# Performance work log

Measured on AMD Instinct MI355X. Metric: run time of the kernel, lower is better.

The kernel has to match this reference:

```python
import jax, jax.numpy as jnp
import numpy as np


def spmm(src, dst, w, x, n):
    # out[i] = sum_{e: dst[e]==i} w[e] * x[src[e]]  == th.spmm(adj, x) with adj COO (dst=row, src=col)
    return jax.ops.segment_sum(x[src] * w[:, None], dst, num_segments=n)


def gcn(x, ei, w, W1, b1, W2, b2):
    # GCN.forward: relu(gc1(x, adj)) -> dropout(eval: identity) -> gc2(x, adj)
    n = x.shape[0]
    src, dst = ei[1], ei[0]
    h = jax.nn.relu(spmm(src, dst, w, x @ W1, n) + b1)
    return spmm(src, dst, w, h @ W2, n) + b2


def setup_inputs() -> dict:
    key = jax.random.key(0)
    ks = jax.random.split(key, 24)
    Nd, Ns = 100000, 50000
    Fd, Fs, H1, H2 = 256, 256, 256, 128
    DEG = 32
    Ed, Es = Nd * DEG, Ns * DEG
    inp = {}
    inp['drug_sim_feat'] = jax.random.normal(ks[0], (Nd, Fd), jnp.float32)
    inp['drug_edge_index'] = jax.random.randint(ks[1], (2, Ed), 0, Nd, jnp.int32)
    inp['drug_edge_weight'] = jax.random.uniform(ks[2], (Ed,), jnp.float32) / DEG
    inp['drug_feat_edge_index'] = jax.random.randint(ks[3], (2, Ed), 0, Nd, jnp.int32)
    inp['drug_feat_edge_weight'] = jax.random.uniform(ks[4], (Ed,), jnp.float32) / DEG
    inp['disease_sim_feat'] = jax.random.normal(ks[5], (Ns, Fs), jnp.float32)
    inp['dis_edge_index'] = jax.random.randint(ks[6], (2, Es), 0, Ns, jnp.int32)
    inp['dis_edge_weight'] = jax.random.uniform(ks[7], (Es,), jnp.float32) / DEG
    inp['dis_feat_edge_index'] = jax.random.randint(ks[8], (2, Es), 0, Ns, jnp.int32)
    inp['dis_feat_edge_weight'] = jax.random.uniform(ks[9], (Es,), jnp.float32) / DEG
    # params: uniform(-stdv, stdv), stdv = 1/sqrt(out_features) as in reset_parameters
    def unif(k, shape, out_f):
        s = 1.0 / np.sqrt(out_f)
        return jax.random.uniform(k, shape, jnp.float32, -s, s)
    inp['W1d'] = unif(ks[10], (Fd, H1), H1); inp['b1d'] = unif(ks[11], (H1,), H1)
    inp['W2d'] = unif(ks[12], (H1, H2), H2); inp['b2d'] = unif(ks[13], (H2,), H2)
    inp['W1s'] = unif(ks[14], (Fs, H1), H1); inp['b1s'] = unif(ks[15], (H1,), H1)
    inp['W2s'] = unif(ks[16], (H1, H2), H2); inp['b2s'] = unif(ks[17], (H2,), H2)
    # fusion Linears (nhid2*2 -> nhid2); kaiming-ish uniform
    fs = 1.0 / np.sqrt(2 * H2)
    inp['Wfd'] = jax.random.uniform(ks[18], (2 * H2, H2), jnp.float32, -fs, fs)
    inp['bfd'] = jax.random.uniform(ks[19], (H2,), jnp.float32, -fs, fs)
    inp['Wfs'] = jax.random.uniform(ks[20], (2 * H2, H2), jnp.float32, -fs, fs)
    inp['bfs'] = jax.random.uniform(ks[21], (H2,), jnp.float32, -fs, fs)
    return inp


def reference(drug_sim_feat, drug_edge_index, drug_edge_weight,
              drug_feat_edge_index, drug_feat_edge_weight,
              disease_sim_feat, dis_edge_index, dis_edge_weight,
              dis_feat_edge_index, dis_feat_edge_weight,
              W1d, b1d, W2d, b2d, W1s, b1s, W2s, b2s,
              Wfd, bfd, Wfs, bfs):
    # dropout in eval mode (identity)
    emb1_sim = gcn(drug_sim_feat, drug_edge_index, drug_edge_weight, W1d, b1d, W2d, b2d)
    emb2_sim = gcn(disease_sim_feat, dis_edge_index, dis_edge_weight, W1s, b1s, W2s, b2s)
    emb1_feat = gcn(drug_sim_feat, drug_feat_edge_index, drug_feat_edge_weight, W1d, b1d, W2d, b2d)
    emb2_feat = gcn(disease_sim_feat, dis_feat_edge_index, dis_feat_edge_weight, W1s, b1s, W2s, b2s)
    emb1 = jax.nn.relu(jnp.concatenate([emb1_sim, emb1_feat], axis=1) @ Wfd + bfd)
    emb2 = jax.nn.relu(jnp.concatenate([emb2_sim, emb2_feat], axis=1) @ Wfs + bfs)
    return (emb1, emb2, emb1_sim, emb1_feat, emb2_sim, emb2_feat)
```

## Files before the change

kernel.cpp:

```cpp
#include <hip/hip_runtime.h>

typedef _Float16 f16;
typedef __attribute__((ext_vector_type(8))) _Float16 f16x8;
typedef __attribute__((ext_vector_type(4))) float f32x4;

__device__ inline ushort f2h_bits(float f) {
    f16 h = (f16)f;
    return __builtin_bit_cast(ushort, h);
}

__global__ __launch_bounds__(256) void f2h_vec(const float* __restrict__ in,
                                               ushort* __restrict__ out, int n4) {
    for (int i = blockIdx.x * 256 + threadIdx.x; i < n4; i += gridDim.x * 256) {
        float4 v = reinterpret_cast<const float4*>(in)[i];
        reinterpret_cast<ushort4*>(out)[i] =
            make_ushort4(f2h_bits(v.x), f2h_bits(v.y), f2h_bits(v.z), f2h_bits(v.w));
    }
}

__global__ __launch_bounds__(256) void transpose_f16_k(const float* __restrict__ W,
                                                       ushort* __restrict__ Wt,
                                                       int K, int N) {
    __shared__ ushort tile[32][33];
    int k0 = blockIdx.x * 32, n0 = blockIdx.y * 32;
    int tx = threadIdx.x & 31, ty = threadIdx.x >> 5;
    #pragma unroll
    for (int i = 0; i < 32; i += 8)
        tile[ty + i][tx] = f2h_bits(W[(size_t)(k0 + ty + i) * N + n0 + tx]);
    __syncthreads();
    #pragma unroll
    for (int i = 0; i < 32; i += 8)
        Wt[(size_t)(n0 + ty + i) * K + k0 + tx] = tile[tx][ty + i];
}


__global__ __launch_bounds__(256) void bucket_hist(const int* __restrict__ dst, int E,
                                                   int* __restrict__ counts) {
    __shared__ int h[512];
    int t = threadIdx.x;
    h[t] = 0; h[t + 256] = 0;
    __syncthreads();
    int e0 = blockIdx.x * 4096;
    #pragma unroll
    for (int k = 0; k < 16; ++k) {
        int i = e0 + t + k * 256;
        if (i < E) atomicAdd(&h[((uint)dst[i]) >> 8], 1);
    }
    __syncthreads();
    for (int b = t; b < 512; b += 256)
        if (h[b]) atomicAdd(&counts[b], h[b]);
}

__global__ __launch_bounds__(256) void bucket_scan(const int* __restrict__ counts, int NB, int E,
                                                   int* __restrict__ base, int* __restrict__ cursor,
                                                   int* __restrict__ row_ptr, int n) {
    int t = threadIdx.x, lane = t & 63, wave = t >> 6;
    int v0 = (2 * t     < NB) ? counts[2 * t]     : 0;
    int v1 = (2 * t + 1 < NB) ? counts[2 * t + 1] : 0;
    int s = v0 + v1;
    int incl = s;
    for (int off = 1; off < 64; off <<= 1) {
        int u = __shfl_up(incl, off);
        if (lane >= off) incl += u;
    }
    __shared__ int wsum[4];
    if (lane == 63) wsum[wave] = incl;
    __syncthreads();
    int excl = incl - s;
    for (int wv = 0; wv < wave; ++wv) excl += wsum[wv];
    if (2 * t < NB)     { base[2 * t]     = excl;      cursor[2 * t]     = excl; }
    if (2 * t + 1 < NB) { base[2 * t + 1] = excl + v0; cursor[2 * t + 1] = excl + v0; }
    if (t == 0) { base[NB] = E; row_ptr[n] = E; }
}

__global__ __launch_bounds__(256) void scatter_binned(const int* __restrict__ ei,
                                                      const float* __restrict__ w, int E,
                                                      int* __restrict__ bucket_cursor,
                                                      int2* __restrict__ bst) {
    __shared__ int hist[512], excl[512], sbase[512], lcur[512];
    __shared__ int2 stage[4096];
    __shared__ ushort sbin[4096];
    const int t = threadIdx.x, lane = t & 63, wave = t >> 6;
    const int e0 = blockIdx.x * 4096;
    const int cnt = min(4096, E - e0);

    hist[t] = 0; hist[t + 256] = 0;
    __syncthreads();

    int   d[16], s[16];
    float wv[16];
    #pragma unroll
    for (int k = 0; k < 16; ++k) {
        int i = t + k * 256;
        if (i < cnt) {
            d[k]  = ei[e0 + i];
            s[k]  = ei[(size_t)E + e0 + i];
            wv[k] = w[e0 + i];
            atomicAdd(&hist[((uint)d[k]) >> 8], 1);
        }
    }
    __syncthreads();

    {
        int v0 = hist[2 * t], v1 = hist[2 * t + 1];
        int sum = v0 + v1;
        int incl = sum;
        for (int off = 1; off < 64; off <<= 1) {
            int u = __shfl_up(incl, off);
            if (lane >= off) incl += u;
        }
        __shared__ int wsum[4];
        if (lane == 63) wsum[wave] = incl;
        __syncthreads();
        int e = incl - sum;
        for (int wvv = 0; wvv < wave; ++wvv) e += wsum[wvv];
        excl[2 * t] = e; excl[2 * t + 1] = e + v0;
    }
    __syncthreads();

    for (int b = t; b < 512; b += 256) {
        int c = hist[b];
        sbase[b] = c ? atomicAdd(&bucket_cursor[b], c) : 0;
        lcur[b] = excl[b];
    }
    __syncthreads();

    #pragma unroll
    for (int k = 0; k < 16; ++k) {
        int i = t + k * 256;
        if (i < cnt) {
            int bin = ((uint)d[k]) >> 8;
            int pos = atomicAdd(&lcur[bin], 1);
            stage[pos] = make_int2((s[k] << 8) | (d[k] & 255), __float_as_int(wv[k]));
            sbin[pos] = (ushort)bin;
        }
    }
    __syncthreads();

    #pragma unroll
    for (int k = 0; k < 16; ++k) {
        int i = t + k * 256;
        if (i < cnt) {
            int2 r = stage[i];
            int bin = sbin[i];
            bst[(size_t)sbase[bin] + i - excl[bin]] = r;
        }
    }
}

__global__ __launch_bounds__(256) void bucket_finalize(const int2* __restrict__ bst,
                                                       const int* __restrict__ base,
                                                       int* __restrict__ row_ptr,
                                                       int2* __restrict__ perm, int n) {
    __shared__ int hist[256], cur[256], wsum[4];
    const int b = blockIdx.x, t = threadIdx.x, lane = t & 63, wave = t >> 6;
    const int lo = base[b], hi = base[b + 1];
    hist[t] = 0;
    __syncthreads();
    for (int i = lo + t; i < hi; i += 256)
        atomicAdd(&hist[bst[i].x & 255], 1);
    __syncthreads();
    int v = hist[t];
    int incl = v;
    for (int off = 1; off < 64; off <<= 1) {
        int u = __shfl_up(incl, off);
        if (lane >= off) incl += u;
    }
    if (lane == 63) wsum[wave] = incl;
    __syncthreads();
    int excl = incl - v;
    for (int wv = 0; wv < wave; ++wv) excl += wsum[wv];
    const int r0 = b << 8;
    const int nrows = min(256, n - r0);
    if (t < nrows) row_ptr[r0 + t] = lo + excl;
    cur[t] = lo + excl;
    __syncthreads();
    for (int i = lo + t; i < hi; i += 256) {
        int2 r = bst[i];
        int local = r.x & 255;
        int slot = atomicAdd(&cur[local], 1);
        perm[slot] = make_int2(r.x >> 8, r.y);
    }
}

template<int C, bool RELU, bool DUAL>
__global__ __launch_bounds__(256) void spmm_f16(
    const f16* __restrict__ x,
    const int2* __restrict__ perm,
    const int* __restrict__ row_ptr, const float* __restrict__ bias,
    ushort* __restrict__ out_h, float* __restrict__ out_f, int n)
{
    const int wave = threadIdx.x >> 6, lane = threadIdx.x & 63;
    const int row = blockIdx.x * 4 + wave;
    if (row >= n) return;
    const int F = 64 * C;
    const int e0 = row_ptr[row], e1 = row_ptr[row + 1];
    float acc[C] = {};
    const int laneoff = lane * C;

    for (int eb = e0; eb < e1; eb += 64) {
        int idx = eb + lane;
        int myS = 0; int myW = 0;
        if (idx < e1) { int2 rec = perm[idx]; myS = rec.x; myW = rec.y; }
        int m = min(64, e1 - eb);
        for (int j0 = 0; j0 < m; j0 += 8) {
            #pragma unroll
            for (int u = 0; u < 8; ++u) {
                int j = j0 + u;
                int   s = __builtin_amdgcn_readlane(myS, j);
                float w = __int_as_float(__builtin_amdgcn_readlane(myW, j));
                const f16* xr = x + (size_t)((uint)s * (uint)F) + laneoff;
                if (C == 4) {
                    union { uint2 u2; f16 h[4]; } cv;
                    cv.u2 = *reinterpret_cast<const uint2*>(xr);
                    acc[0] = fmaf((float)cv.h[0], w, acc[0]);
                    acc[1] = fmaf((float)cv.h[1], w, acc[1]);
                    acc[2] = fmaf((float)cv.h[2], w, acc[2]);
                    acc[3] = fmaf((float)cv.h[3], w, acc[3]);
                } else {
                    union { uint u1; f16 h[2]; } cv;
                    cv.u1 = *reinterpret_cast<const uint*>(xr);
                    acc[0] = fmaf((float)cv.h[0], w, acc[0]);
                    acc[1] = fmaf((float)cv.h[1], w, acc[1]);
                }
            }
        }
    }

    #pragma unroll
    for (int c = 0; c < C; ++c) {
        float v = acc[c] + bias[laneoff + c];
        acc[c] = RELU ? fmaxf(v, 0.f) : v;
    }
    size_t ob = (size_t)row * F + laneoff;
    if (DUAL) {
        if (C == 4) *reinterpret_cast<float4*>(out_f + ob) = make_float4(acc[0], acc[1], acc[2], acc[3]);
        else        *reinterpret_cast<float2*>(out_f + ob) = make_float2(acc[0], acc[1]);
    }
    if (C == 4) *reinterpret_cast<ushort4*>(out_h + ob) =
        make_ushort4(f2h_bits(acc[0]), f2h_bits(acc[1]), f2h_bits(acc[2]), f2h_bits(acc[3]));
    else        *reinterpret_cast<ushort2*>(out_h + ob) =
        make_ushort2(f2h_bits(acc[0]), f2h_bits(acc[1]));
}

template<bool FUSE, bool RELU, bool BIAS, bool F32OUT>
__global__ __launch_bounds__(256) void gemm_mfma(
    const ushort* __restrict__ A, const ushort* __restrict__ A2,
    const ushort* __restrict__ Bt, const float* __restrict__ bias,
    ushort* __restrict__ Ch, float* __restrict__ Cf,
    int M, int N, int K)
{
    __shared__ ushort Asb[128 * 32];
    __shared__ ushort Bsb[128 * 32];
    const int tid = threadIdx.x;
    const int lane = tid & 63, wave = tid >> 6;
    const int wr = wave >> 1, wc = wave & 1;
    const int bm = blockIdx.x * 128, bn = blockIdx.y * 128;

    f32x4 acc[4][4] = {};

    for (int k0 = 0; k0 < K; k0 += 32) {
        #pragma unroll
        for (int h = 0; h < 2; ++h) {
            int slot = tid + 256 * h;
            int r = slot >> 2, cb = slot & 3;
            int row = bm + r;
            uint4 v = make_uint4(0, 0, 0, 0);
            if (row < M) {
                int kk = k0 + cb * 8;
                if (FUSE) {
                    const ushort* Ap = (kk < 128) ? A : A2;
                    v = *reinterpret_cast<const uint4*>(Ap + (size_t)row * 128 + (kk & 127));
                } else {
                    v = *reinterpret_cast<const uint4*>(A + (size_t)row * K + kk);
                }
            }
            int scb = cb ^ ((r >> 1) & 3);
            *reinterpret_cast<uint4*>(&Asb[r * 32 + scb * 8]) = v;
        }
        #pragma unroll
        for (int h = 0; h < 2; ++h) {
            int slot = tid + 256 * h;
            int r = slot >> 2, cb = slot & 3;
            uint4 v = *reinterpret_cast<const uint4*>(Bt + (size_t)(bn + r) * K + k0 + cb * 8);
            int scb = cb ^ ((r >> 1) & 3);
            *reinterpret_cast<uint4*>(&Bsb[r * 32 + scb * 8]) = v;
        }
        __syncthreads();

        f16x8 fa[4], fb[4];
        #pragma unroll
        for (int i = 0; i < 4; ++i) {
            int r = wr * 64 + i * 16 + (lane & 15);
            int scb = (lane >> 4) ^ ((r >> 1) & 3);
            fa[i] = *reinterpret_cast<const f16x8*>(&Asb[r * 32 + scb * 8]);
        }
        #pragma unroll
        for (int j = 0; j < 4; ++j) {
            int r = wc * 64 + j * 16 + (lane & 15);
            int scb = (lane >> 4) ^ ((r >> 1) & 3);
            fb[j] = *reinterpret_cast<const f16x8*>(&Bsb[r * 32 + scb * 8]);
        }
        #pragma unroll
        for (int i = 0; i < 4; ++i)
            #pragma unroll
            for (int j = 0; j < 4; ++j)
                acc[i][j] = __builtin_amdgcn_mfma_f32_16x16x32_f16(fa[i], fb[j], acc[i][j], 0, 0, 0);
        __syncthreads();
    }

    #pragma unroll
    for (int i = 0; i < 4; ++i) {
        #pragma unroll
        for (int r4 = 0; r4 < 4; ++r4) {
            int row = bm + wr * 64 + i * 16 + (lane >> 4) * 4 + r4;
            if (row >= M) continue;
            #pragma unroll
            for (int j = 0; j < 4; ++j) {
                int col = bn + wc * 64 + j * 16 + (lane & 15);
                float v = acc[i][j][r4];
                if (BIAS) v += bias[col];
                if (RELU) v = fmaxf(v, 0.f);
                if (F32OUT) Cf[(size_t)row * N + col] = v;
                else        Ch[(size_t)row * N + col] = f2h_bits(v);
            }
        }
    }
}

extern "C" void kernel_launch(void* const* d_in, const int* in_sizes, int n_in,
                              void* d_out, int out_size, void* d_ws, size_t ws_size,
                              hipStream_t stream) {
    const float* Xd       = (const float*)d_in[0];
    const int*   eid_sim  = (const int*)  d_in[1];
    const float* wd_sim   = (const float*)d_in[2];
    const int*   eid_feat = (const int*)  d_in[3];
    const float* wd_feat  = (const float*)d_in[4];
    const float* Xs       = (const float*)d_in[5];
    const int*   eis_sim  = (const int*)  d_in[6];
    const float* ws_sim   = (const float*)d_in[7];
    const int*   eis_feat = (const int*)  d_in[8];
    const float* ws_feat  = (const float*)d_in[9];
    const float* W1d = (const float*)d_in[10]; const float* b1d = (const float*)d_in[11];
    const float* W2d = (const float*)d_in[12]; const float* b2d = (const float*)d_in[13];
    const float* W1s = (const float*)d_in[14]; const float* b1s = (const float*)d_in[15];
    const float* W2s = (const float*)d_in[16]; const float* b2s = (const float*)d_in[17];
    const float* Wfd = (const float*)d_in[18]; const float* bfd = (const float*)d_in[19];
    const float* Wfs = (const float*)d_in[20]; const float* bfs = (const float*)d_in[21];

    const int Fd = 256, H1 = 256, H2 = 128;
    const int Nd = in_sizes[0] / Fd;
    const int Ns = in_sizes[5] / Fd;
    const int Ed = in_sizes[2];
    const int Es = in_sizes[7];

    float* out    = (float*)d_out;
    float* o_emb1 = out;
    float* o_emb2 = o_emb1 + (size_t)Nd * H2;
    float* o_e1s  = o_emb2 + (size_t)Ns * H2;
    float* o_e1f  = o_e1s  + (size_t)Nd * H2;
    float* o_e2s  = o_e1f  + (size_t)Nd * H2;
    float* o_e2f  = o_e2s  + (size_t)Ns * H2;

    char* p = (char*)d_ws;
    auto alloc = [&](size_t bytes) { char* q = p; p += (bytes + 255) & ~(size_t)255; return q; };
    ushort* x_h   = (ushort*)alloc((size_t)Nd * 256 * 2);
    ushort* xw1   = (ushort*)alloc((size_t)Nd * 256 * 2);
    ushort* hbuf  = (ushort*)alloc((size_t)Nd * 256 * 2);
    ushort* tbuf  = (ushort*)alloc((size_t)Nd * 128 * 2);
    ushort* es_h  = (ushort*)alloc((size_t)Nd * 128 * 2);
    ushort* ef_h  = (ushort*)alloc((size_t)Nd * 128 * 2);
    ushort* W1dt  = (ushort*)alloc(256 * 256 * 2);
    ushort* W2dt  = (ushort*)alloc(256 * 128 * 2);
    ushort* Wfdt  = (ushort*)alloc(256 * 128 * 2);
    ushort* W1st  = (ushort*)alloc(256 * 256 * 2);
    ushort* W2st  = (ushort*)alloc(256 * 128 * 2);
    ushort* Wfst  = (ushort*)alloc(256 * 128 * 2);
    int2*   perm     = (int2*)alloc((size_t)Ed * 8);
    int*    row_ptr  = (int*) alloc((size_t)(Nd + 1) * 4);
    int*    bcounts  = (int*) alloc(512 * 4);
    int*    bbase    = (int*) alloc(513 * 4);
    int*    bcursor  = (int*) alloc(512 * 4);
    int2*   bst      = (int2*)hbuf;

    transpose_f16_k<<<dim3(8, 8), 256, 0, stream>>>(W1d, W1dt, 256, 256);
    transpose_f16_k<<<dim3(8, 4), 256, 0, stream>>>(W2d, W2dt, 256, 128);
    transpose_f16_k<<<dim3(8, 4), 256, 0, stream>>>(Wfd, Wfdt, 256, 128);
    transpose_f16_k<<<dim3(8, 8), 256, 0, stream>>>(W1s, W1st, 256, 256);
    transpose_f16_k<<<dim3(8, 4), 256, 0, stream>>>(W2s, W2st, 256, 128);
    transpose_f16_k<<<dim3(8, 4), 256, 0, stream>>>(Wfs, Wfst, 256, 128);

    auto branch = [&](const float* X, int n,
                      const int* ei1, const float* w1,
                      const int* ei2, const float* w2, int E,
                      const ushort* W1t, const float* b1,
                      const ushort* W2t, const float* b2,
                      const ushort* Wft, const float* bfu,
                      float* o_sim, float* o_feat, float* o_emb) {
        const int NB = (n + 255) >> 8;
        const int EB = (E + 4095) / 4096;
        f2h_vec<<<2048, 256, 0, stream>>>(X, x_h, n * 64);
        gemm_mfma<false, false, false, false><<<dim3((n + 127) / 128, 2), 256, 0, stream>>>(
            x_h, nullptr, W1t, nullptr, xw1, nullptr, n, 256, 256);
        const int*   eis[2]  = {ei1, ei2};
        const float* wss[2]  = {w1, w2};
        float*       of[2]   = {o_sim, o_feat};
        ushort*      oh[2]   = {es_h, ef_h};
        for (int g = 0; g < 2; ++g) {
            hipMemsetAsync(bcounts, 0, 512 * 4, stream);
            bucket_hist<<<EB, 256, 0, stream>>>(eis[g], E, bcounts);
            bucket_scan<<<1, 256, 0, stream>>>(bcounts, NB, E, bbase, bcursor, row_ptr, n);
            scatter_binned<<<EB, 256, 0, stream>>>(eis[g], wss[g], E, bcursor, bst);
            bucket_finalize<<<NB, 256, 0, stream>>>(bst, bbase, row_ptr, perm, n);
            spmm_f16<4, true, false><<<(n + 3) / 4, 256, 0, stream>>>(
                (const f16*)xw1, perm, row_ptr, b1, hbuf, nullptr, n);
            gemm_mfma<false, false, false, false><<<dim3((n + 127) / 128, 1), 256, 0, stream>>>(
                hbuf, nullptr, W2t, nullptr, tbuf, nullptr, n, 128, 256);
            spmm_f16<2, false, true><<<(n + 3) / 4, 256, 0, stream>>>(
                (const f16*)tbuf, perm, row_ptr, b2, oh[g], of[g], n);
        }
        gemm_mfma<true, true, true, true><<<dim3((n + 127) / 128, 1), 256, 0, stream>>>(
            es_h, ef_h, Wft, bfu, nullptr, o_emb, n, 128, 256);
    };

    branch(Xd, Nd, eid_sim, wd_sim, eid_feat, wd_feat, Ed,
           W1dt, b1d, W2dt, b2d, Wfdt, bfd, o_e1s, o_e1f, o_emb1);
    branch(Xs, Ns, eis_sim, ws_sim, eis_feat, ws_feat, Es,
           W1st, b1s, W2st, b2s, Wfst, bfs, o_e2s, o_e2f, o_emb2);
}
```

Before: 1.505 ms.

## Batch CSR build for all four graphs and fuse fp16 conversion into GEMM

The histogram, scan, scatter and finalize stages now run once for all four graphs, using a blockIdx.y graph index and per-graph descriptors, instead of four separate sequences. This cuts kernel launches and lets the small stages fill the device. The six weight transposes become one launch, and the f2h conversion pass is folded into the first GEMM's A-tile load, so the half-precision copy of X is never written or reread. In exchange, permutation and row_ptr buffers are now kept for every graph, which uses more workspace, and the staging area is reused from the xw1 buffer.

After: 1.384 ms. 8.0% less time.

```diff
diff --git a/kernel.cpp b/kernel.cpp
--- a/kernel.cpp
+++ b/kernel.cpp
@@ -9,20 +9,20 @@
     return __builtin_bit_cast(ushort, h);
 }
 
-__global__ __launch_bounds__(256) void f2h_vec(const float* __restrict__ in,
-                                               ushort* __restrict__ out, int n4) {
-    for (int i = blockIdx.x * 256 + threadIdx.x; i < n4; i += gridDim.x * 256) {
-        float4 v = reinterpret_cast<const float4*>(in)[i];
-        reinterpret_cast<ushort4*>(out)[i] =
-            make_ushort4(f2h_bits(v.x), f2h_bits(v.y), f2h_bits(v.z), f2h_bits(v.w));
-    }
-}
-
-__global__ __launch_bounds__(256) void transpose_f16_k(const float* __restrict__ W,
-                                                       ushort* __restrict__ Wt,
-                                                       int K, int N) {
+struct T6 {
+    const float* s[6];
+    ushort* d[6];
+    int N[6];
+};
+
+__global__ __launch_bounds__(256) void transpose6_k(T6 a) {
     __shared__ ushort tile[32][33];
+    const int z = blockIdx.z;
+    const int K = 256, N = a.N[z];
     int k0 = blockIdx.x * 32, n0 = blockIdx.y * 32;
+    if (n0 >= N) return;
+    const float* W = a.s[z];
+    ushort* Wt = a.d[z];
     int tx = threadIdx.x & 31, ty = threadIdx.x >> 5;
     #pragma unroll
     for (int i = 0; i < 32; i += 8)
@@ -33,30 +33,43 @@
         Wt[(size_t)(n0 + ty + i) * K + k0 + tx] = tile[tx][ty + i];
 }
 
-
-__global__ __launch_bounds__(256) void bucket_hist(const int* __restrict__ dst, int E,
-                                                   int* __restrict__ counts) {
+struct GraphDesc {
+    const int* ei;
+    const float* w;
+    int E, n, NB, bstoff;
+    int* row_ptr;
+    int2* perm;
+};
+struct G4 { GraphDesc g[4]; };
+
+__global__ __launch_bounds__(256) void hist_b(G4 a, int* __restrict__ bcounts) {
+    const GraphDesc& G = a.g[blockIdx.y];
+    const int e0 = blockIdx.x * 4096;
+    if (e0 >= G.E) return;
     __shared__ int h[512];
     int t = threadIdx.x;
     h[t] = 0; h[t + 256] = 0;
     __syncthreads();
-    int e0 = blockIdx.x * 4096;
     #pragma unroll
     for (int k = 0; k < 16; ++k) {
         int i = e0 + t + k * 256;
-        if (i < E) atomicAdd(&h[((uint)dst[i]) >> 8], 1);
-    }
-    __syncthreads();
+        if (i < G.E) atomicAdd(&h[((uint)G.ei[i]) >> 8], 1);
+    }
+    __syncthreads();
+    int* bc = bcounts + blockIdx.y * 512;
     for (int b = t; b < 512; b += 256)
-        if (h[b]) atomicAdd(&counts[b], h[b]);
-}
-
-__global__ __launch_bounds__(256) void bucket_scan(const int* __restrict__ counts, int NB, int E,
-                                                   int* __restrict__ base, int* __restrict__ cursor,
-                                                   int* __restrict__ row_ptr, int n) {
+        if (h[b]) atomicAdd(&bc[b], h[b]);
+}
+
+__global__ __launch_bounds__(256) void scan_b(G4 a, const int* __restrict__ bcounts,
+                                              int* __restrict__ bbase, int* __restrict__ bcursor) {
+    const int gidx = blockIdx.x;
+    const GraphDesc& G = a.g[gidx];
+    const int* bc = bcounts + gidx * 512;
+    int* base = bbase + gidx * 513;
+    int* cur  = bcursor + gidx * 512;
     int t = threadIdx.x, lane = t & 63, wave = t >> 6;
-    int v0 = (2 * t     < NB) ? counts[2 * t]     : 0;
-    int v1 = (2 * t + 1 < NB) ? counts[2 * t + 1] : 0;
+    int v0 = bc[2 * t], v1 = bc[2 * t + 1];
     int s = v0 + v1;
     int incl = s;
     for (int off = 1; off < 64; off <<= 1) {
@@ -68,21 +81,22 @@
     __syncthreads();
     int excl = incl - s;
     for (int wv = 0; wv < wave; ++wv) excl += wsum[wv];
-    if (2 * t < NB)     { base[2 * t]     = excl;      cursor[2 * t]     = excl; }
-    if (2 * t + 1 < NB) { base[2 * t + 1] = excl + v0; cursor[2 * t + 1] = excl + v0; }
-    if (t == 0) { base[NB] = E; row_ptr[n] = E; }
-}
-
-__global__ __launch_bounds__(256) void scatter_binned(const int* __restrict__ ei,
-                                                      const float* __restrict__ w, int E,
-                                                      int* __restrict__ bucket_cursor,
-                                                      int2* __restrict__ bst) {
+    base[2 * t] = excl;      cur[2 * t] = excl;
+    base[2 * t + 1] = excl + v0; cur[2 * t + 1] = excl + v0;
+    if (t == 0) { base[512] = G.E; G.row_ptr[G.n] = G.E; }
+}
+
+__global__ __launch_bounds__(256) void scatter_b(G4 a, int* __restrict__ bcursor,
+                                                 int2* __restrict__ bst) {
+    const GraphDesc& G = a.g[blockIdx.y];
+    const int e0 = blockIdx.x * 4096;
+    if (e0 >= G.E) return;
     __shared__ int hist[512], excl[512], sbase[512], lcur[512];
     __shared__ int2 stage[4096];
     __shared__ ushort sbin[4096];
     const int t = threadIdx.x, lane = t & 63, wave = t >> 6;
-    const int e0 = blockIdx.x * 4096;
-    const int cnt = min(4096, E - e0);
+    const int cnt = min(4096, G.E - e0);
+    int* bcur = bcursor + blockIdx.y * 512;
 
     hist[t] = 0; hist[t + 256] = 0;
     __syncthreads();
@@ -93,9 +107,9 @@
     for (int k = 0; k < 16; ++k) {
         int i = t + k * 256;
         if (i < cnt) {
-            d[k]  = ei[e0 + i];
-            s[k]  = ei[(size_t)E + e0 + i];
-            wv[k] = w[e0 + i];
+            d[k]  = G.ei[e0 + i];
+            s[k]  = G.ei[(size_t)G.E + e0 + i];
+            wv[k] = G.w[e0 + i];
             atomicAdd(&hist[((uint)d[k]) >> 8], 1);
         }
     }
@@ -120,7 +134,7 @@
 
     for (int b = t; b < 512; b += 256) {
         int c = hist[b];
-        sbase[b] = c ? atomicAdd(&bucket_cursor[b], c) : 0;
+        sbase[b] = c ? atomicAdd(&bcur[b], c) : 0;
         lcur[b] = excl[b];
     }
     __syncthreads();
@@ -143,22 +157,25 @@
         if (i < cnt) {
             int2 r = stage[i];
             int bin = sbin[i];
-            bst[(size_t)sbase[bin] + i - excl[bin]] = r;
-        }
-    }
-}
-
-__global__ __launch_bounds__(256) void bucket_finalize(const int2* __restrict__ bst,
-                                                       const int* __restrict__ base,
-                                                       int* __restrict__ row_ptr,
-                                                       int2* __restrict__ perm, int n) {
+            bst[(size_t)G.bstoff + sbase[bin] + i - excl[bin]] = r;
+        }
+    }
+}
+
+__global__ __launch_bounds__(256) void finalize_b(G4 a, const int* __restrict__ bbase,
+                                                  const int2* __restrict__ bst) {
+    const GraphDesc& G = a.g[blockIdx.y];
+    const int b = blockIdx.x;
+    if (b >= G.NB) return;
     __shared__ int hist[256], cur[256], wsum[4];
-    const int b = blockIdx.x, t = threadIdx.x, lane = t & 63, wave = t >> 6;
+    const int t = threadIdx.x, lane = t & 63, wave = t >> 6;
+    const int* base = bbase + blockIdx.y * 513;
     const int lo = base[b], hi = base[b + 1];
+    const int2* bg = bst + G.bstoff;
     hist[t] = 0;
     __syncthreads();
     for (int i = lo + t; i < hi; i += 256)
-        atomicAdd(&hist[bst[i].x & 255], 1);
+        atomicAdd(&hist[bg[i].x & 255], 1);
     __syncthreads();
     int v = hist[t];
     int incl = v;
@@ -171,15 +188,15 @@
     int excl = incl - v;
     for (int wv = 0; wv < wave; ++wv) excl += wsum[wv];
     const int r0 = b << 8;
-    const int nrows = min(256, n - r0);
-    if (t < nrows) row_ptr[r0 + t] = lo + excl;
+    const int nrows = min(256, G.n - r0);
+    if (t < nrows) G.row_ptr[r0 + t] = lo + excl;
     cur[t] = lo + excl;
     __syncthreads();
     for (int i = lo + t; i < hi; i += 256) {
-        int2 r = bst[i];
+        int2 r = bg[i];
         int local = r.x & 255;
         int slot = atomicAdd(&cur[local], 1);
-        perm[slot] = make_int2(r.x >> 8, r.y);
+        G.perm[slot] = make_int2(r.x >> 8, r.y);
     }
 }
 
@@ -243,9 +260,9 @@
         make_ushort2(f2h_bits(acc[0]), f2h_bits(acc[1]));
 }
 
-template<bool FUSE, bool RELU, bool BIAS, bool F32OUT>
+template<bool CVTA, bool FUSE, bool RELU, bool BIAS, bool F32OUT>
 __global__ __launch_bounds__(256) void gemm_mfma(
-    const ushort* __restrict__ A, const ushort* __restrict__ A2,
+    const void* __restrict__ Av, const ushort* __restrict__ A2,
     const ushort* __restrict__ Bt, const float* __restrict__ bias,
     ushort* __restrict__ Ch, float* __restrict__ Cf,
     int M, int N, int K)
@@ -268,11 +285,18 @@
             uint4 v = make_uint4(0, 0, 0, 0);
             if (row < M) {
                 int kk = k0 + cb * 8;
-                if (FUSE) {
-                    const ushort* Ap = (kk < 128) ? A : A2;
+                if (CVTA) {
+                    const float* Af = (const float*)Av;
+                    float4 lo = *reinterpret_cast<const float4*>(Af + (size_t)row * K + kk);
+                    float4 hi = *reinterpret_cast<const float4*>(Af + (size_t)row * K + kk + 4);
+                    ushort h8[8] = { f2h_bits(lo.x), f2h_bits(lo.y), f2h_bits(lo.z), f2h_bits(lo.w),
+                                     f2h_bits(hi.x), f2h_bits(hi.y), f2h_bits(hi.z), f2h_bits(hi.w) };
+                    v = *reinterpret_cast<const uint4*>(h8);
+                } else if (FUSE) {
+                    const ushort* Ap = (kk < 128) ? (const ushort*)Av : A2;
                     v = *reinterpret_cast<const uint4*>(Ap + (size_t)row * 128 + (kk & 127));
                 } else {
-                    v = *reinterpret_cast<const uint4*>(A + (size_t)row * K + kk);
+                    v = *reinterpret_cast<const uint4*>((const ushort*)Av + (size_t)row * K + kk);
                 }
             }
             int scb = cb ^ ((r >> 1) & 3);
@@ -364,7 +388,6 @@
 
     char* p = (char*)d_ws;
     auto alloc = [&](size_t bytes) { char* q = p; p += (bytes + 255) & ~(size_t)255; return q; };
-    ushort* x_h   = (ushort*)alloc((size_t)Nd * 256 * 2);
     ushort* xw1   = (ushort*)alloc((size_t)Nd * 256 * 2);
     ushort* hbuf  = (ushort*)alloc((size_t)Nd * 256 * 2);
     ushort* tbuf  = (ushort*)alloc((size_t)Nd * 128 * 2);
@@ -376,55 +399,69 @@
     ushort* W1st  = (ushort*)alloc(256 * 256 * 2);
     ushort* W2st  = (ushort*)alloc(256 * 128 * 2);
     ushort* Wfst  = (ushort*)alloc(256 * 128 * 2);
-    int2*   perm     = (int2*)alloc((size_t)Ed * 8);
-    int*    row_ptr  = (int*) alloc((size_t)(Nd + 1) * 4);
-    int*    bcounts  = (int*) alloc(512 * 4);
-    int*    bbase    = (int*) alloc(513 * 4);
-    int*    bcursor  = (int*) alloc(512 * 4);
-    int2*   bst      = (int2*)hbuf;
-
-    transpose_f16_k<<<dim3(8, 8), 256, 0, stream>>>(W1d, W1dt, 256, 256);
-    transpose_f16_k<<<dim3(8, 4), 256, 0, stream>>>(W2d, W2dt, 256, 128);
-    transpose_f16_k<<<dim3(8, 4), 256, 0, stream>>>(Wfd, Wfdt, 256, 128);
-    transpose_f16_k<<<dim3(8, 8), 256, 0, stream>>>(W1s, W1st, 256, 256);
-    transpose_f16_k<<<dim3(8, 4), 256, 0, stream>>>(W2s, W2st, 256, 128);
-    transpose_f16_k<<<dim3(8, 4), 256, 0, stream>>>(Wfs, Wfst, 256, 128);
+    int2*   perm0 = (int2*)alloc((size_t)Ed * 8);
+    int2*   perm1 = (int2*)alloc((size_t)Ed * 8);
+    int2*   perm2 = (int2*)alloc((size_t)Es * 8);
+    int2*   perm3 = (int2*)alloc((size_t)Es * 8);
+    int*    rp0   = (int*) alloc((size_t)(Nd + 1) * 4);
+    int*    rp1   = (int*) alloc((size_t)(Nd + 1) * 4);
+    int*    rp2   = (int*) alloc((size_t)(Ns + 1) * 4);
+    int*    rp3   = (int*) alloc((size_t)(Ns + 1) * 4);
+    int*    bcounts = (int*)alloc(4 * 512 * 4);
+    int*    bbase   = (int*)alloc(4 * 513 * 4);
+    int*    bcursor = (int*)alloc(4 * 512 * 4);
+    int2*   bst     = (int2*)xw1;
+
+    {
+        T6 a;
+        a.s[0] = W1d; a.s[1] = W2d; a.s[2] = Wfd; a.s[3] = W1s; a.s[4] = W2s; a.s[5] = Wfs;
+        a.d[0] = W1dt; a.d[1] = W2dt; a.d[2] = Wfdt; a.d[3] = W1st; a.d[4] = W2st; a.d[5] = Wfst;
+        a.N[0] = 256; a.N[1] = 128; a.N[2] = 128; a.N[3] = 256; a.N[4] = 128; a.N[5] = 128;
+        transpose6_k<<<dim3(8, 8, 6), 256, 0, stream>>>(a);
+    }
+
+    G4 a;
+    a.g[0] = { eid_sim,  wd_sim,  Ed, Nd, (Nd + 255) >> 8, 0,           rp0, perm0 };
+    a.g[1] = { eid_feat, wd_feat, Ed, Nd, (Nd + 255) >> 8, Ed,          rp1, perm1 };
+    a.g[2] = { eis_sim,  ws_sim,  Es, Ns, (Ns + 255) >> 8, 2 * Ed,      rp2, perm2 };
+    a.g[3] = { eis_feat, ws_feat, Es, Ns, (Ns + 255) >> 8, 2 * Ed + Es, rp3, perm3 };
+    {
+        const int maxEB = (Ed + 4095) / 4096;
+        const int maxNB = (Nd + 255) >> 8;
+        hipMemsetAsync(bcounts, 0, 4 * 512 * 4, stream);
+        hist_b<<<dim3(maxEB, 4), 256, 0, stream>>>(a, bcounts);
+        scan_b<<<4, 256, 0, stream>>>(a, bcounts, bbase, bcursor);
+        scatter_b<<<dim3(maxEB, 4), 256, 0, stream>>>(a, bcursor, bst);
+        finalize_b<<<dim3(maxNB, 4), 256, 0, stream>>>(a, bbase, bst);
+    }
 
     auto branch = [&](const float* X, int n,
-                      const int* ei1, const float* w1,
-                      const int* ei2, const float* w2, int E,
+                      const int2* pA, const int* rpA,
+                      const int2* pB, const int* rpB,
                       const ushort* W1t, const float* b1,
                       const ushort* W2t, const float* b2,
                       const ushort* Wft, const float* bfu,
                       float* o_sim, float* o_feat, float* o_emb) {
-        const int NB = (n + 255) >> 8;
-        const int EB = (E + 4095) / 4096;
-        f2h_vec<<<2048, 256, 0, stream>>>(X, x_h, n * 64);
-        gemm_mfma<false, false, false, false><<<dim3((n + 127) / 128, 2), 256, 0, stream>>>(
-            x_h, nullptr, W1t, nullptr, xw1, nullptr, n, 256, 256);
-        const int*   eis[2]  = {ei1, ei2};
-        const float* wss[2]  = {w1, w2};
-        float*       of[2]   = {o_sim, o_feat};
-        ushort*      oh[2]   = {es_h, ef_h};
+        gemm_mfma<true, false, false, false, false><<<dim3((n + 127) / 128, 2), 256, 0, stream>>>(
+            X, nullptr, W1t, nullptr, xw1, nullptr, n, 256, 256);
+        const int2* pm[2] = {pA, pB};
+        const int*  rp[2] = {rpA, rpB};
+        float*      of[2] = {o_sim, o_feat};
+        ushort*     oh[2] = {es_h, ef_h};
         for (int g = 0; g < 2; ++g) {
-            hipMemsetAsync(bcounts, 0, 512 * 4, stream);
-            bucket_hist<<<EB, 256, 0, stream>>>(eis[g], E, bcounts);
-            bucket_scan<<<1, 256, 0, stream>>>(bcounts, NB, E, bbase, bcursor, row_ptr, n);
-            scatter_binned<<<EB, 256, 0, stream>>>(eis[g], wss[g], E, bcursor, bst);
-            bucket_finalize<<<NB, 256, 0, stream>>>(bst, bbase, row_ptr, perm, n);
             spmm_f16<4, true, false><<<(n + 3) / 4, 256, 0, stream>>>(
-                (const f16*)xw1, perm, row_ptr, b1, hbuf, nullptr, n);
-            gemm_mfma<false, false, false, false><<<dim3((n + 127) / 128, 1), 256, 0, stream>>>(
+                (const f16*)xw1, pm[g], rp[g], b1, hbuf, nullptr, n);
+            gemm_mfma<false, false, false, false, false><<<dim3((n + 127) / 128, 1), 256, 0, stream>>>(
                 hbuf, nullptr, W2t, nullptr, tbuf, nullptr, n, 128, 256);
             spmm_f16<2, false, true><<<(n + 3) / 4, 256, 0, stream>>>(
-                (const f16*)tbuf, perm, row_ptr, b2, oh[g], of[g], n);
-        }
-        gemm_mfma<true, true, true, true><<<dim3((n + 127) / 128, 1), 256, 0, stream>>>(
+                (const f16*)tbuf, pm[g], rp[g], b2, oh[g], of[g], n);
+        }
+        gemm_mfma<false, true, true, true, true><<<dim3((n + 127) / 128, 1), 256, 0, stream>>>(
             es_h, ef_h, Wft, bfu, nullptr, o_emb, n, 128, 256);
     };
 
-    branch(Xd, Nd, eid_sim, wd_sim, eid_feat, wd_feat, Ed,
+    branch(Xd, Nd, perm0, rp0, perm1, rp1,
            W1dt, b1d, W2dt, b2d, Wfdt, bfd, o_e1s, o_e1f, o_emb1);
-    branch(Xs, Ns, eis_sim, ws_sim, eis_feat, ws_feat, Es,
+    branch(Xs, Ns, perm2, rp2, perm3, rp3,
            W1st, b1s, W2st, b2s, Wfst, bfs, o_e2s, o_e2f, o_emb2);
 }
```
